# Performance work log

Hardware: AMD Instinct MI355X
Metric: run time of the kernel (lower is better)

The kernel has to match this reference:

```python
import jax, jax.numpy as jnp
import numpy as np

VEC_DIM = 128
N_DOCS = 100000
N_WORDS = 100000
BATCH = 16384
CTX = 8
N_SAMPLES = 6


def setup_inputs() -> dict:
    key = jax.random.key(0)
    k1, k2, k3, k4, k5 = jax.random.split(key, 5)
    doc_ids = jax.random.randint(k1, (BATCH,), 0, N_DOCS, dtype=jnp.int64 if jax.config.jax_enable_x64 else jnp.int32)
    context_ids = jax.random.randint(k2, (BATCH, CTX), 0, N_WORDS)
    sample_ids = jax.random.randint(k3, (BATCH, N_SAMPLES), 0, N_WORDS)
    paragraph_matrix = jax.random.normal(k4, (N_DOCS, VEC_DIM), dtype=jnp.float32)
    word_matrix = jax.random.normal(k5, (N_WORDS, VEC_DIM), dtype=jnp.float32)
    outputs = jnp.zeros((VEC_DIM, N_WORDS), dtype=jnp.float32)
    return {
        "doc_ids": doc_ids,
        "context_ids": context_ids,
        "sample_ids": sample_ids,
        "paragraph_matrix": paragraph_matrix,
        "word_matrix": word_matrix,
        "outputs": outputs,
    }


def reference(doc_ids, context_ids, sample_ids, paragraph_matrix, word_matrix, outputs):
    # concat=False branch of DistributedMemory.forward
    # [B, CTX, D] gathered then summed over context -> [B, D]
    word_sum = jnp.sum(word_matrix[context_ids, :], axis=1)
    doc_vec = paragraph_matrix[doc_ids, :]            # [B, D]
    inputs = doc_vec + word_sum                       # [B, D]
    # outputs[:, sample_ids] -> [D, B, S]; bmm([B,1,D],[B,D,S]) == einsum
    out_cols = outputs[:, sample_ids]                 # [D, B, S]
    logits = jnp.einsum("bd,dbs->bs", inputs, out_cols)  # [B, S]
    return logits
```

## Files before the change

kernel.cpp:

```cpp
#include <hip/hip_runtime.h>
#include <stdint.h>

#define VEC_DIM   128
#define N_WORDS   100000
#define CTX       8
#define N_SAMPLES 6
#define BATCH     16384
#define N_GROUPS  6250
#define TOTAL_S   (BATCH * N_SAMPLES)

static constexpr size_t OFF_INPUTS  = 0;
static constexpr size_t OFF_HIST    = 8388608;
static constexpr size_t OFF_OFFS    = OFF_HIST   + 25024;
static constexpr size_t OFF_CURSOR  = OFF_OFFS   + 25088;
static constexpr size_t OFF_RECORDS = OFF_CURSOR + 25024;

__global__ void k_zero(uint32_t* hist) {
    int i = blockIdx.x * 256 + threadIdx.x;
    if (i < N_GROUPS) hist[i] = 0u;
}

__global__ __launch_bounds__(256) void k_gather_inputs(
    const int* __restrict__ doc_ids, const int* __restrict__ context_ids,
    const float* __restrict__ para, const float* __restrict__ words,
    float* __restrict__ inputs)
{
    const int wave = threadIdx.x >> 6;
    const int lane = threadIdx.x & 63;
    const int b    = blockIdx.x * 4 + wave;

    const int doc = doc_ids[b];
    int cids[CTX];
    #pragma unroll
    for (int c = 0; c < CTX; ++c) cids[c] = context_ids[b * CTX + c];

    const float2* prow = reinterpret_cast<const float2*>(para + (size_t)doc * VEC_DIM);
    float2 acc = prow[lane];
    #pragma unroll
    for (int c = 0; c < CTX; ++c) {
        const float2* wrow = reinterpret_cast<const float2*>(words + (size_t)cids[c] * VEC_DIM);
        float2 w = wrow[lane];
        acc.x += w.x; acc.y += w.y;
    }
    reinterpret_cast<float2*>(inputs)[(size_t)b * 64 + lane] = acc;
}

__global__ void k_hist(const int* __restrict__ sample_ids, uint32_t* __restrict__ hist) {
    int i = blockIdx.x * 256 + threadIdx.x;
    int id = sample_ids[i];
    atomicAdd(&hist[id >> 4], 1u);
}

__global__ __launch_bounds__(256) void k_scan(const uint32_t* __restrict__ hist,
                                              uint32_t* __restrict__ offs,
                                              uint32_t* __restrict__ cursor)
{
    __shared__ uint32_t part[256];
    const int t = threadIdx.x;
    const int CHUNK = 25;
    const int base = t * CHUNK;

    uint32_t s = 0;
    for (int k = 0; k < CHUNK; ++k) {
        int g = base + k;
        if (g < N_GROUPS) s += hist[g];
    }
    part[t] = s;
    __syncthreads();
    if (t == 0) {
        uint32_t run = 0;
        for (int i = 0; i < 256; ++i) { uint32_t v = part[i]; part[i] = run; run += v; }
        offs[N_GROUPS] = run;
    }
    __syncthreads();
    uint32_t run = part[t];
    for (int k = 0; k < CHUNK; ++k) {
        int g = base + k;
        if (g < N_GROUPS) {
            offs[g]   = run;
            cursor[g] = run;
            run += hist[g];
        }
    }
}

__global__ void k_scatter(const int* __restrict__ sample_ids,
                          uint32_t* __restrict__ cursor,
                          uint64_t* __restrict__ records)
{
    int i = blockIdx.x * 256 + threadIdx.x;
    int id = sample_ids[i];
    int g  = id >> 4;
    uint32_t pos = atomicAdd(&cursor[g], 1u);
    int b = i / N_SAMPLES;
    int s = i - b * N_SAMPLES;
    records[pos] = ((uint64_t)(uint32_t)(b * 8 + s) << 32) | (uint32_t)id;
}

__global__ __launch_bounds__(256) void k_process(
    const float* __restrict__ outs,
    const float* __restrict__ inputs,
    const uint32_t* __restrict__ offs,
    const uint64_t* __restrict__ records,
    float* __restrict__ logits)
{
    const int g = blockIdx.x;
    const uint32_t begin = offs[g];
    const uint32_t end   = offs[g + 1];
    if (begin == end) return;

    __shared__ float tile[VEC_DIM][17];

    const int t = threadIdx.x;
    const int base_col = g * 16;
    #pragma unroll
    for (int k = 0; k < 8; ++k) {
        int idx = t + k * 256;
        int d = idx >> 4, c = idx & 15;
        tile[d][c] = outs[(size_t)d * N_WORDS + base_col + c];
    }
    __syncthreads();

    const int wave = t >> 6;
    const int lane = t & 63;
    const float2* inputs2 = reinterpret_cast<const float2*>(inputs);

    for (uint32_t i = begin + wave; i < end; i += 4) {
        uint64_t rec = records[i];
        int bs = (int)(rec >> 32);
        int c  = (int)(rec & 15u);
        int b  = bs >> 3;

        float2 v = inputs2[(size_t)b * 64 + lane];
        float p = v.x * tile[2 * lane][c] + v.y * tile[2 * lane + 1][c];
        #pragma unroll
        for (int off = 32; off > 0; off >>= 1)
            p += __shfl_xor(p, off, 64);
        if (lane == 0)
            logits[(size_t)b * N_SAMPLES + (bs & 7)] = p;
    }
}

extern "C" void kernel_launch(void* const* d_in, const int* in_sizes, int n_in,
                              void* d_out, int out_size, void* d_ws, size_t ws_size,
                              hipStream_t stream) {
    const int*   doc_ids     = (const int*)  d_in[0];
    const int*   context_ids = (const int*)  d_in[1];
    const int*   sample_ids  = (const int*)  d_in[2];
    const float* para        = (const float*)d_in[3];
    const float* words       = (const float*)d_in[4];
    const float* outs        = (const float*)d_in[5];
    float*       logits      = (float*)      d_out;

    char* ws = (char*)d_ws;
    float*    inputs  = (float*)   (ws + OFF_INPUTS);
    uint32_t* hist    = (uint32_t*)(ws + OFF_HIST);
    uint32_t* offs    = (uint32_t*)(ws + OFF_OFFS);
    uint32_t* cursor  = (uint32_t*)(ws + OFF_CURSOR);
    uint64_t* records = (uint64_t*)(ws + OFF_RECORDS);

    hipLaunchKernelGGL(k_zero, dim3((N_GROUPS + 255) / 256), dim3(256), 0, stream, hist);
    hipLaunchKernelGGL(k_gather_inputs, dim3(BATCH / 4), dim3(256), 0, stream,
                       doc_ids, context_ids, para, words, inputs);
    hipLaunchKernelGGL(k_hist, dim3(TOTAL_S / 256), dim3(256), 0, stream, sample_ids, hist);
    hipLaunchKernelGGL(k_scan, dim3(1), dim3(256), 0, stream, hist, offs, cursor);
    hipLaunchKernelGGL(k_scatter, dim3(TOTAL_S / 256), dim3(256), 0, stream,
                       sample_ids, cursor, records);
    hipLaunchKernelGGL(k_process, dim3(N_GROUPS), dim3(256), 0, stream,
                       outs, inputs, offs, records, logits);
}
```

Before: 206.7 us.

## Fuse histogram into gather, parallelize scan, use 16-lane dot products in process

Folds the sample-id histogram into the input-gather kernel so one launch goes away. It also replaces the serial single-thread prefix over partial sums with a parallel Hillis-Steele scan that keeps histogram values in registers. The process kernel stores the output tile transposed and computes each dot product with 16 lanes using float4 loads, so a wave handles four records per step instead of one. The trade-off is more registers in the scan and a different LDS access pattern for the tile.

```diff
diff --git a/kernel.cpp b/kernel.cpp
--- a/kernel.cpp
+++ b/kernel.cpp
@@ -20,14 +20,21 @@
     if (i < N_GROUPS) hist[i] = 0u;
 }
 
-__global__ __launch_bounds__(256) void k_gather_inputs(
+__global__ __launch_bounds__(256) void k_gather_hist(
     const int* __restrict__ doc_ids, const int* __restrict__ context_ids,
+    const int* __restrict__ sample_ids,
     const float* __restrict__ para, const float* __restrict__ words,
-    float* __restrict__ inputs)
+    float* __restrict__ inputs, uint32_t* __restrict__ hist)
 {
-    const int wave = threadIdx.x >> 6;
-    const int lane = threadIdx.x & 63;
+    const int t    = threadIdx.x;
+    const int wave = t >> 6;
+    const int lane = t & 63;
     const int b    = blockIdx.x * 4 + wave;
+
+    if (t < 24) {
+        int id = sample_ids[blockIdx.x * 24 + t];
+        atomicAdd(&hist[id >> 4], 1u);
+    }
 
     const int doc = doc_ids[b];
     int cids[CTX];
@@ -45,12 +52,6 @@
     reinterpret_cast<float2*>(inputs)[(size_t)b * 64 + lane] = acc;
 }
 
-__global__ void k_hist(const int* __restrict__ sample_ids, uint32_t* __restrict__ hist) {
-    int i = blockIdx.x * 256 + threadIdx.x;
-    int id = sample_ids[i];
-    atomicAdd(&hist[id >> 4], 1u);
-}
-
 __global__ __launch_bounds__(256) void k_scan(const uint32_t* __restrict__ hist,
                                               uint32_t* __restrict__ offs,
                                               uint32_t* __restrict__ cursor)
@@ -60,26 +61,31 @@
     const int CHUNK = 25;
     const int base = t * CHUNK;
 
+    uint32_t h[CHUNK];
     uint32_t s = 0;
     for (int k = 0; k < CHUNK; ++k) {
         int g = base + k;
-        if (g < N_GROUPS) s += hist[g];
+        h[k] = (g < N_GROUPS) ? hist[g] : 0u;
+        s += h[k];
     }
     part[t] = s;
     __syncthreads();
-    if (t == 0) {
-        uint32_t run = 0;
-        for (int i = 0; i < 256; ++i) { uint32_t v = part[i]; part[i] = run; run += v; }
-        offs[N_GROUPS] = run;
+    #pragma unroll
+    for (int off = 1; off < 256; off <<= 1) {
+        uint32_t v = part[t];
+        if (t >= off) v += part[t - off];
+        __syncthreads();
+        part[t] = v;
+        __syncthreads();
     }
-    __syncthreads();
-    uint32_t run = part[t];
+    uint32_t run = (t == 0) ? 0u : part[t - 1];
+    if (t == 0) offs[N_GROUPS] = TOTAL_S;
     for (int k = 0; k < CHUNK; ++k) {
         int g = base + k;
         if (g < N_GROUPS) {
             offs[g]   = run;
             cursor[g] = run;
-            run += hist[g];
+            run += h[k];
         }
     }
 }
@@ -109,7 +115,7 @@
     const uint32_t end   = offs[g + 1];
     if (begin == end) return;
 
-    __shared__ float tile[VEC_DIM][17];
+    __shared__ float tileT[16][132];
 
     const int t = threadIdx.x;
     const int base_col = g * 16;
@@ -117,26 +123,33 @@
     for (int k = 0; k < 8; ++k) {
         int idx = t + k * 256;
         int d = idx >> 4, c = idx & 15;
-        tile[d][c] = outs[(size_t)d * N_WORDS + base_col + c];
+        tileT[c][d] = outs[(size_t)d * N_WORDS + base_col + c];
     }
     __syncthreads();
 
-    const int wave = t >> 6;
-    const int lane = t & 63;
-    const float2* inputs2 = reinterpret_cast<const float2*>(inputs);
+    const int slot = t >> 4;
+    const int j    = t & 15;
 
-    for (uint32_t i = begin + wave; i < end; i += 4) {
+    for (uint32_t i = begin + slot; i < end; i += 16) {
         uint64_t rec = records[i];
         int bs = (int)(rec >> 32);
         int c  = (int)(rec & 15u);
         int b  = bs >> 3;
 
-        float2 v = inputs2[(size_t)b * 64 + lane];
-        float p = v.x * tile[2 * lane][c] + v.y * tile[2 * lane + 1][c];
+        const float4* inp4 = reinterpret_cast<const float4*>(inputs + (size_t)b * VEC_DIM);
+        float4 a0 = inp4[j * 2];
+        float4 a1 = inp4[j * 2 + 1];
+        float4 w0 = *reinterpret_cast<const float4*>(&tileT[c][j * 8]);
+        float4 w1 = *reinterpret_cast<const float4*>(&tileT[c][j * 8 + 4]);
+
+        float p = a0.x * w0.x + a0.y * w0.y + a0.z * w0.z + a0.w * w0.w
+                + a1.x * w1.x + a1.y * w1.y + a1.z * w1.z + a1.w * w1.w;
+
         #pragma unroll
-        for (int off = 32; off > 0; off >>= 1)
+        for (int off = 1; off < 16; off <<= 1)
             p += __shfl_xor(p, off, 64);
-        if (lane == 0)
+
+        if (j == 0)
             logits[(size_t)b * N_SAMPLES + (bs & 7)] = p;
     }
 }
@@ -160,9 +173,8 @@
     uint64_t* records = (uint64_t*)(ws + OFF_RECORDS);
 
     hipLaunchKernelGGL(k_zero, dim3((N_GROUPS + 255) / 256), dim3(256), 0, stream, hist);
-    hipLaunchKernelGGL(k_gather_inputs, dim3(BATCH / 4), dim3(256), 0, stream,
-                       doc_ids, context_ids, para, words, inputs);
-    hipLaunchKernelGGL(k_hist, dim3(TOTAL_S / 256), dim3(256), 0, stream, sample_ids, hist);
+    hipLaunchKernelGGL(k_gather_hist, dim3(BATCH / 4), dim3(256), 0, stream,
+                       doc_ids, context_ids, sample_ids, para, words, inputs, hist);
     hipLaunchKernelGGL(k_scan, dim3(1), dim3(256), 0, stream, hist, offs, cursor);
     hipLaunchKernelGGL(k_scatter, dim3(TOTAL_S / 256), dim3(256), 0, stream,
                        sample_ids, cursor, records);
```

After: 188.0 us. -9.0%, faster.
